# Kernel tuning notes

Hardware: AMD Instinct MI355X
Metric: run time of the kernel (lower is better)

## Reference

```python
import jax, jax.numpy as jnp
import numpy as np

TEMPERATURE = 0.07
EPS = 1e-12  # F.normalize default eps

def _l2norm(x):
    n = jnp.linalg.norm(x, axis=1, keepdims=True)
    return x / jnp.maximum(n, EPS)

def setup_inputs() -> dict:
    key = jax.random.key(0)
    k1, k2 = jax.random.split(key)
    N, D = 16384, 256
    return {
        "feat_local": jax.random.normal(k1, (N, D), dtype=jnp.float32),
        "feat_global": jax.random.normal(k2, (N, D), dtype=jnp.float32),
    }

def reference(feat_local, feat_global):
    fl = _l2norm(feat_local)
    fg = _l2norm(feat_global)
    # [N, N] similarity matrix scaled by temperature
    sim = jnp.einsum('nd,md->nm', fl, fg) / TEMPERATURE
    pos_sim = jnp.diagonal(sim)
    loss = -pos_sim + jax.scipy.special.logsumexp(sim, axis=1)
    return loss.mean()
```

## Files before the change

kernel.cpp:

```cpp
#include <hip/hip_runtime.h>
#include <hip/hip_bf16.h>

#define NROWS 16384
#define DIM   256
#define DB    (DIM / 2)
#define SEGS  8
#define BN    128
#define TB    (BN * DB)
#define NT    ((NROWS / SEGS) / BN)
#define INVT  14.285714285714286f
#define C1f   20.60992915555662f
#define LN2f  0.6931471805599453f

typedef __attribute__((ext_vector_type(8)))  int   int8v;
typedef __attribute__((ext_vector_type(16))) float f32x16;

#define SCA 0x7F7F7F7Fu
#define SCB 0x7B7B7B7Bu

__device__ __forceinline__ unsigned fp4q(float v) {
    float a = fabsf(v);
    unsigned s = (__float_as_uint(v) >> 28) & 0x8u;
    unsigned idx = (unsigned)(a >= 0.25f) + (a >= 0.75f) + (a >= 1.25f) + (a >= 1.75f)
                 + (a >= 2.5f) + (a >= 3.5f) + (a >= 5.0f);
    return s | idx;
}

__global__ __launch_bounds__(256) void norm_diag_kernel(
    const float* __restrict__ fl, const float* __restrict__ fg,
    unsigned char* __restrict__ A, unsigned char* __restrict__ B,
    float* __restrict__ diag, float* __restrict__ out)
{
    int tid  = threadIdx.x;
    int wave = tid >> 6, lane = tid & 63;
    int row  = blockIdx.x * 4 + wave;
    if (blockIdx.x == 0 && tid == 0) out[0] = 0.0f;

    float4 xl = ((const float4*)(fl + (size_t)row * DIM))[lane];
    float4 xg = ((const float4*)(fg + (size_t)row * DIM))[lane];
    float ssl = xl.x*xl.x + xl.y*xl.y + xl.z*xl.z + xl.w*xl.w;
    float ssg = xg.x*xg.x + xg.y*xg.y + xg.z*xg.z + xg.w*xg.w;
    for (int m = 1; m < 64; m <<= 1) {
        ssl += __shfl_xor(ssl, m, 64);
        ssg += __shfl_xor(ssg, m, 64);
    }
    float il = 1.0f / fmaxf(sqrtf(ssl), 1e-12f);
    float ig = 1.0f / fmaxf(sqrtf(ssg), 1e-12f);
    float nl0 = xl.x*il, nl1 = xl.y*il, nl2 = xl.z*il, nl3 = xl.w*il;
    float ng0 = xg.x*ig, ng1 = xg.y*ig, ng2 = xg.z*ig, ng3 = xg.w*ig;

    unsigned pa4 = fp4q(nl0 * C1f) | (fp4q(nl1 * C1f) << 4)
                 | (fp4q(nl2 * C1f) << 8) | (fp4q(nl3 * C1f) << 12);
    ((unsigned short*)(A + (size_t)row * DB))[lane] = (unsigned short)pa4;

    unsigned pb4 = fp4q(ng0 * 16.0f) | (fp4q(ng1 * 16.0f) << 4)
                 | (fp4q(ng2 * 16.0f) << 8) | (fp4q(ng3 * 16.0f) << 12);
    {
        int kcb4 = lane >> 3;
        unsigned chunk = (unsigned)((row >> 7) * 1024 + ((row >> 6) & 1) * 512
                                    + kcb4 * 64 + (row & 63));
        ((unsigned short*)B)[chunk * 8 + (lane & 7)] = (unsigned short)pb4;
    }

    float d = nl0*ng0 + nl1*ng1 + nl2*ng2 + nl3*ng3;
    for (int m = 1; m < 64; m <<= 1) d += __shfl_xor(d, m, 64);
    if (lane == 0) diag[row] = d;
}

__global__ __launch_bounds__(256, 4) void sim_lse_kernel(
    const unsigned char* __restrict__ A, const unsigned char* __restrict__ B,
    float* __restrict__ lpart)
{
    __shared__ __align__(16) unsigned char bt[2 * TB];

    int tid  = threadIdx.x;
    int lane = tid & 63;
    int l31  = lane & 31, half = lane >> 5;
    int wave = tid >> 6;
    int seg  = blockIdx.x;
    int rowBase = blockIdx.y * 128 + wave * 32;

    unsigned vb = (unsigned)(l31 * 16 + half * 1024);

    const int4 zero4 = make_int4(0, 0, 0, 0);

    int8v af[4];
    {
        const unsigned char* ap = A + (size_t)(rowBase + l31) * DB + half * 16;
#pragma unroll
        for (int kk = 0; kk < 4; ++kk) {
            ((int4*)&af[kk])[0] = *(const int4*)(ap + kk * 32);
            ((int4*)&af[kk])[1] = zero4;
        }
    }

    f32x16 lv;
    f32x16 accA, accB;
#pragma unroll
    for (int r = 0; r < 16; ++r) {
        lv[r] = -1.0f;
        accB[r] = 0.0f;
    }

    int T0 = seg * NT;

    auto stage = [&](int T, unsigned bufo) {
        const unsigned char* g = B + (size_t)T * TB + (unsigned)tid * 16;
        unsigned lo = bufo + (unsigned)tid * 16;
#pragma unroll
        for (int j = 0; j < 4; ++j) {
            __builtin_amdgcn_global_load_lds(
                (const __attribute__((address_space(1))) unsigned int*)(g + j * 4096),
                (__attribute__((address_space(3))) unsigned int*)&bt[lo + j * 4096],
                16, 0, 0);
        }
    };

#define MFMA4(dst, a, b, cin) \
    dst = __builtin_amdgcn_mfma_scale_f32_32x32x64_f8f6f4(a, b, cin, 4, 4, 0, SCA, 0, SCB)

    auto unit = [&](f32x16& ac, f32x16& ax, unsigned ab, unsigned offc) {
#pragma unroll
        for (int r = 0; r < 16; ++r) ac[r] = 0.0f;
        int8v b0, b1;
        ((int4*)&b0)[1] = zero4; ((int4*)&b1)[1] = zero4;
        ((int4*)&b0)[0] = *(const int4*)&bt[ab + offc];
        ((int4*)&b1)[0] = *(const int4*)&bt[ab + offc + 2048u];
        MFMA4(ac, af[0], b0, ac);
        ((int4*)&b0)[0] = *(const int4*)&bt[ab + offc + 4096u];
        MFMA4(ac, af[1], b1, ac);
#pragma unroll
        for (int r = 0; r < 8; ++r)
            lv[r] += __builtin_amdgcn_exp2f(ax[r]);
        ((int4*)&b1)[0] = *(const int4*)&bt[ab + offc + 6144u];
        MFMA4(ac, af[2], b0, ac);
        MFMA4(ac, af[3], b1, ac);
#pragma unroll
        for (int r = 8; r < 16; ++r)
            lv[r] += __builtin_amdgcn_exp2f(ax[r]);
    };

    stage(T0, 0);

    for (int t = 0; t < NT; ++t) {
        unsigned bufo = (t & 1) ? (unsigned)TB : 0u;
        __syncthreads();

        if (t + 1 < NT)
            stage(T0 + t + 1, (t & 1) ? 0u : (unsigned)TB);

        unsigned ab = vb + bufo;
        unit(accA, accB, ab, 0u);
        unit(accB, accA, ab, 512u);
        unit(accA, accB, ab, 8192u);
        unit(accB, accA, ab, 8704u);
    }
#pragma unroll
    for (int r = 0; r < 16; ++r)
        lv[r] += __builtin_amdgcn_exp2f(accB[r]);

#pragma unroll
    for (int r = 0; r < 16; ++r) {
        float v = lv[r];
        v += __shfl_xor(v, 1, 64);
        v += __shfl_xor(v, 2, 64);
        v += __shfl_xor(v, 4, 64);
        v += __shfl_xor(v, 8, 64);
        v += __shfl_xor(v, 16, 64);
        lv[r] = v;
    }
    if (l31 == 0) {
#pragma unroll
        for (int r = 0; r < 16; ++r) {
            int row = rowBase + (r & 3) + 8*(r >> 2) + 4*half;
            lpart[(size_t)seg * NROWS + row] = lv[r];
        }
    }
#undef MFMA4
}

__global__ __launch_bounds__(256) void reduce_kernel(
    const float* __restrict__ lpart, const float* __restrict__ diag,
    float* __restrict__ out)
{
    __shared__ float sm[4];
    int gtid = blockIdx.x * 256 + threadIdx.x;
    float s = 0.0f;
    for (int row = gtid; row < NROWS; row += 32 * 256) {
        float t = 0.0f;
#pragma unroll
        for (int g = 0; g < SEGS; ++g) t += lpart[(size_t)g * NROWS + row];
        s += LN2f * log2f(t) - INVT * diag[row];
    }
    for (int m = 1; m < 64; m <<= 1) s += __shfl_xor(s, m, 64);
    int wave = threadIdx.x >> 6, lane = threadIdx.x & 63;
    if (lane == 0) sm[wave] = s;
    __syncthreads();
    if (threadIdx.x == 0) {
        float tot = sm[0] + sm[1] + sm[2] + sm[3];
        atomicAdd(out, tot * (1.0f / NROWS));
    }
}

extern "C" void kernel_launch(void* const* d_in, const int* in_sizes, int n_in,
                              void* d_out, int out_size, void* d_ws, size_t ws_size,
                              hipStream_t stream) {
    const float* fl = (const float*)d_in[0];
    const float* fg = (const float*)d_in[1];
    float* out = (float*)d_out;

    char* ws = (char*)d_ws;
    unsigned char* A = (unsigned char*)ws;
    unsigned char* B = A + (size_t)NROWS * DB;
    float* diag  = (float*)(ws + 2 * (size_t)NROWS * DB);
    float* lpart = diag + NROWS;

    norm_diag_kernel<<<NROWS / 4, 256, 0, stream>>>(fl, fg, A, B, diag, out);
    sim_lse_kernel<<<dim3(SEGS, NROWS / 128), 256, 0, stream>>>(A, B, lpart);
    reduce_kernel<<<32, 256, 0, stream>>>(lpart, diag, out);
}
```

Before: 123.3 us.

## Interleave two independent MFMA chains per slot and rebalance column segments

```diff
diff --git a/kernel.cpp b/kernel.cpp
--- a/kernel.cpp
+++ b/kernel.cpp
@@ -4,10 +4,9 @@
 #define NROWS 16384
 #define DIM   256
 #define DB    (DIM / 2)
-#define SEGS  8
+#define SEGS  6
 #define BN    128
 #define TB    (BN * DB)
-#define NT    ((NROWS / SEGS) / BN)
 #define INVT  14.285714285714286f
 #define C1f   20.60992915555662f
 #define LN2f  0.6931471805599453f
@@ -67,7 +66,7 @@
     if (lane == 0) diag[row] = d;
 }
 
-__global__ __launch_bounds__(256, 4) void sim_lse_kernel(
+__global__ __launch_bounds__(256, 3) void sim_lse_kernel(
     const unsigned char* __restrict__ A, const unsigned char* __restrict__ B,
     float* __restrict__ lpart)
 {
@@ -78,6 +77,8 @@
     int l31  = lane & 31, half = lane >> 5;
     int wave = tid >> 6;
     int seg  = blockIdx.x;
+    int nt   = 21 + (seg < 2 ? 1 : 0);
+    int T0   = seg * 21 + (seg < 2 ? seg : 2);
     int rowBase = blockIdx.y * 128 + wave * 32;
 
     unsigned vb = (unsigned)(l31 * 16 + half * 1024);
@@ -95,14 +96,12 @@
     }
 
     f32x16 lv;
-    f32x16 accA, accB;
+    f32x16 p0, p1, q0, q1;
 #pragma unroll
     for (int r = 0; r < 16; ++r) {
-        lv[r] = -1.0f;
-        accB[r] = 0.0f;
-    }
-
-    int T0 = seg * NT;
+        lv[r] = -2.0f;
+        q0[r] = 0.0f; q1[r] = 0.0f;
+    }
 
     auto stage = [&](int T, unsigned bufo) {
         const unsigned char* g = B + (size_t)T * TB + (unsigned)tid * 16;
@@ -119,45 +118,55 @@
 #define MFMA4(dst, a, b, cin) \
     dst = __builtin_amdgcn_mfma_scale_f32_32x32x64_f8f6f4(a, b, cin, 4, 4, 0, SCA, 0, SCB)
 
-    auto unit = [&](f32x16& ac, f32x16& ax, unsigned ab, unsigned offc) {
-#pragma unroll
-        for (int r = 0; r < 16; ++r) ac[r] = 0.0f;
-        int8v b0, b1;
+    auto slot = [&](f32x16& c0, f32x16& c1, f32x16& e0, f32x16& e1,
+                    unsigned ab, unsigned offA, unsigned offB) {
+#pragma unroll
+        for (int r = 0; r < 16; ++r) { c0[r] = 0.0f; c1[r] = 0.0f; }
+        int8v b0, b1, b2, b3;
         ((int4*)&b0)[1] = zero4; ((int4*)&b1)[1] = zero4;
-        ((int4*)&b0)[0] = *(const int4*)&bt[ab + offc];
-        ((int4*)&b1)[0] = *(const int4*)&bt[ab + offc + 2048u];
-        MFMA4(ac, af[0], b0, ac);
-        ((int4*)&b0)[0] = *(const int4*)&bt[ab + offc + 4096u];
-        MFMA4(ac, af[1], b1, ac);
-#pragma unroll
-        for (int r = 0; r < 8; ++r)
-            lv[r] += __builtin_amdgcn_exp2f(ax[r]);
-        ((int4*)&b1)[0] = *(const int4*)&bt[ab + offc + 6144u];
-        MFMA4(ac, af[2], b0, ac);
-        MFMA4(ac, af[3], b1, ac);
-#pragma unroll
-        for (int r = 8; r < 16; ++r)
-            lv[r] += __builtin_amdgcn_exp2f(ax[r]);
+        ((int4*)&b2)[1] = zero4; ((int4*)&b3)[1] = zero4;
+        ((int4*)&b0)[0] = *(const int4*)&bt[ab + offA];
+        ((int4*)&b1)[0] = *(const int4*)&bt[ab + offB];
+        MFMA4(c0, af[0], b0, c0);
+        MFMA4(c1, af[0], b1, c1);
+#pragma unroll
+        for (int r = 0; r < 8; ++r)  lv[r] += __builtin_amdgcn_exp2f(e0[r]);
+        ((int4*)&b2)[0] = *(const int4*)&bt[ab + offA + 2048u];
+        ((int4*)&b3)[0] = *(const int4*)&bt[ab + offB + 2048u];
+        MFMA4(c0, af[1], b2, c0);
+        MFMA4(c1, af[1], b3, c1);
+#pragma unroll
+        for (int r = 8; r < 16; ++r) lv[r] += __builtin_amdgcn_exp2f(e0[r]);
+        ((int4*)&b0)[0] = *(const int4*)&bt[ab + offA + 4096u];
+        ((int4*)&b1)[0] = *(const int4*)&bt[ab + offB + 4096u];
+        MFMA4(c0, af[2], b0, c0);
+        MFMA4(c1, af[2], b1, c1);
+#pragma unroll
+        for (int r = 0; r < 8; ++r)  lv[r] += __builtin_amdgcn_exp2f(e1[r]);
+        ((int4*)&b2)[0] = *(const int4*)&bt[ab + offA + 6144u];
+        ((int4*)&b3)[0] = *(const int4*)&bt[ab + offB + 6144u];
+        MFMA4(c0, af[3], b2, c0);
+        MFMA4(c1, af[3], b3, c1);
+#pragma unroll
+        for (int r = 8; r < 16; ++r) lv[r] += __builtin_amdgcn_exp2f(e1[r]);
     };
 
     stage(T0, 0);
 
-    for (int t = 0; t < NT; ++t) {
+    for (int t = 0; t < nt; ++t) {
         unsigned bufo = (t & 1) ? (unsigned)TB : 0u;
         __syncthreads();
 
-        if (t + 1 < NT)
+        if (t + 1 < nt)
             stage(T0 + t + 1, (t & 1) ? 0u : (unsigned)TB);
 
         unsigned ab = vb + bufo;
-        unit(accA, accB, ab, 0u);
-        unit(accB, accA, ab, 512u);
-        unit(accA, accB, ab, 8192u);
-        unit(accB, accA, ab, 8704u);
+        slot(p0, p1, q0, q1, ab, 0u,    512u);
+        slot(q0, q1, p0, p1, ab, 8192u, 8704u);
     }
 #pragma unroll
     for (int r = 0; r < 16; ++r)
-        lv[r] += __builtin_amdgcn_exp2f(accB[r]);
+        lv[r] += __builtin_amdgcn_exp2f(q0[r]) + __builtin_amdgcn_exp2f(q1[r]);
 
 #pragma unroll
     for (int r = 0; r < 16; ++r) {
```

Result: no change. 122.8 us (-0.4%).
